# Optimization experiments

Measured on AMD Instinct MI355X. Metric: run time of the kernel, lower is better.

## Reference

```python
import jax, jax.numpy as jnp
import numpy as np

N_NODES = 50000
N_EDGES = 800000
IN_C, HID_C, OUT_C = 256, 128, 64
NUM_LAYERS = 3


def _glorot(key, shape):
    fan_in, fan_out = shape[0], shape[1]
    lim = np.sqrt(6.0 / (fan_in + fan_out)).astype(np.float32)
    return jax.random.uniform(key, shape, jnp.float32, -lim, lim)


def setup_inputs() -> dict:
    key = jax.random.key(0)
    ks = jax.random.split(key, 16)
    inp = {
        "x": jax.random.normal(ks[0], (N_NODES, IN_C), jnp.float32),
        "edge_index": jax.random.randint(ks[1], (2, N_EDGES), 0, N_NODES, jnp.int64),
        "proj_W": _glorot(ks[2], (IN_C, HID_C)),
        "proj_b": jnp.zeros((HID_C,), jnp.float32),
        "conv_W0": _glorot(ks[3], (HID_C, HID_C)),
        "conv_b0": jnp.zeros((HID_C,), jnp.float32),
        "conv_W1": _glorot(ks[4], (HID_C, HID_C)),
        "conv_b1": jnp.zeros((HID_C,), jnp.float32),
        "conv_W2": _glorot(ks[5], (HID_C, HID_C)),
        "conv_b2": jnp.zeros((HID_C,), jnp.float32),
        "out_W": _glorot(ks[6], (HID_C, OUT_C)),
        "out_b": jnp.zeros((OUT_C,), jnp.float32),
    }
    return inp


def _gcn_conv(h, W, b, src, dst, norm):
    # GCNConv: transform, then normalized scatter-add aggregation (self-loops
    # are already folded into src/dst/norm).
    h = h @ W                                   # [N, hid]
    msg = h[src] * norm[:, None]                # [E+N, hid] gather + scale
    agg = jax.ops.segment_sum(msg, dst, num_segments=N_NODES)
    return agg + b


def reference(x, edge_index, proj_W, proj_b, conv_W0, conv_b0, conv_W1,
              conv_b1, conv_W2, conv_b2, out_W, out_b):
    # Add self-loops once (same structure every layer).
    loop = jnp.arange(N_NODES, dtype=edge_index.dtype)
    src = jnp.concatenate([edge_index[0], loop])
    dst = jnp.concatenate([edge_index[1], loop])
    # Symmetric normalization: deg computed on destinations incl. self-loops.
    deg = jax.ops.segment_sum(jnp.ones_like(dst, dtype=x.dtype), dst,
                              num_segments=N_NODES)
    dis = jnp.where(deg > 0, jax.lax.rsqrt(deg), 0.0)
    norm = dis[src] * dis[dst]

    h = x @ proj_W + proj_b
    for W, b in ((conv_W0, conv_b0), (conv_W1, conv_b1), (conv_W2, conv_b2)):
        h = jax.nn.relu(_gcn_conv(h, W, b, src, dst, norm))
        # dropout is identity in eval mode
    return h @ out_W + out_b
```

## Files before the change

### kernel.cpp

```cpp
#include <hip/hip_runtime.h>
#include <hip/hip_bf16.h>

#define N_NODES 50000
#define N_EDGES 800000
#define IN_C 256
#define HID_C 128
#define OUT_C 64

#define N_BINS ((N_NODES + 127) / 128)
#define N_TOT (N_EDGES + N_NODES)

#define RB_BLOCK 1024
#define RB_EPT 8
#define RB_CHUNK (RB_BLOCK * RB_EPT)
#define RB_GRID ((N_TOT + RB_CHUNK - 1) / RB_CHUNK)

typedef __attribute__((ext_vector_type(8))) short bf16x8;
typedef __attribute__((ext_vector_type(4))) float f32x4;
typedef __attribute__((ext_vector_type(2))) _Float16 f16x2;

__device__ __forceinline__ ushort f2bf(float f) {
    uint u = __float_as_uint(f);
    u += 0x7fff + ((u >> 16) & 1);
    return (ushort)(u >> 16);
}
__device__ __forceinline__ float bf2f(ushort h) {
    return __uint_as_float(((uint)h) << 16);
}
__device__ __forceinline__ uint packhl(float v) {
    ushort h = f2bf(v);
    ushort l = f2bf(v - bf2f(h));
    return ((uint)h << 16) | (uint)l;
}


__global__ __launch_bounds__(256) void zero_binhist_kernel(int* __restrict__ binhist) {
    int i = blockIdx.x * 256 + threadIdx.x;
    if (i < N_BINS) binhist[i] = 0;
}

__global__ __launch_bounds__(256) void bin_hist_kernel(const int* __restrict__ dst,
                                                       int* __restrict__ binhist) {
    __shared__ int h[N_BINS];
    int t = threadIdx.x;
    for (int b = t; b < N_BINS; b += 256) h[b] = 0;
    __syncthreads();
    for (int i = blockIdx.x * 256 + t; i < N_EDGES; i += gridDim.x * 256)
        atomicAdd(&h[dst[i] >> 7], 1);
    __syncthreads();
    for (int b = t; b < N_BINS; b += 256)
        if (h[b]) atomicAdd(&binhist[b], h[b]);
}

__global__ __launch_bounds__(512) void bin_scan_kernel(const int* __restrict__ binhist,
                                                       int* __restrict__ bin_base,
                                                       int* __restrict__ bincur,
                                                       int* __restrict__ row_ptr) {
    __shared__ int s[512];
    int t = threadIdx.x;
    int v = 0;
    if (t < N_BINS) {
        int sl = (t == N_BINS - 1) ? (N_NODES - (N_BINS - 1) * 128) : 128;
        v = binhist[t] + sl;
    }
    s[t] = v;
    __syncthreads();
    for (int off = 1; off < 512; off <<= 1) {
        int x = s[t];
        int a = (t >= off) ? s[t - off] : 0;
        __syncthreads();
        s[t] = x + a;
        __syncthreads();
    }
    if (t < N_BINS) {
        bin_base[t] = s[t] - v;
        bincur[t] = 0;
    }
    if (t == N_BINS - 1) bin_base[N_BINS] = s[t];
    if (t == 0) row_ptr[N_NODES] = N_TOT;
}

__global__ __launch_bounds__(RB_BLOCK) void bin_scatter_kernel(
    const int* __restrict__ src, const int* __restrict__ dst,
    const int* __restrict__ bin_base, int* __restrict__ bincur,
    uint* __restrict__ binned) {
    __shared__ int hist[N_BINS];
    __shared__ int cur[N_BINS];
    const int t = threadIdx.x;
    for (int b = t; b < N_BINS; b += RB_BLOCK) hist[b] = 0;
    __syncthreads();

    uint pk[RB_EPT];
    int bn[RB_EPT];
    const int base = blockIdx.x * RB_CHUNK;
#pragma unroll
    for (int k = 0; k < RB_EPT; k++) {
        int i = base + k * RB_BLOCK + t;
        bn[k] = -1;
        if (i < N_TOT) {
            int s, d;
            if (i < N_EDGES) {
                s = src[i];
                d = dst[i];
            } else {
                s = d = i - N_EDGES;
            }
            pk[k] = (uint)s | ((uint)d << 16);
            bn[k] = d >> 7;
            atomicAdd(&hist[bn[k]], 1);
        }
    }
    __syncthreads();

    for (int b = t; b < N_BINS; b += RB_BLOCK) {
        int c = hist[b];
        int g0 = (c > 0) ? atomicAdd(&bincur[b], c) : 0;
        cur[b] = bin_base[b] + g0;
    }
    __syncthreads();

#pragma unroll
    for (int k = 0; k < RB_EPT; k++) {
        if (bn[k] >= 0) {
            int pos = atomicAdd(&cur[bn[k]], 1);
            binned[pos] = pk[k];
        }
    }
}

__global__ __launch_bounds__(256) void csr_build_kernel(const uint* __restrict__ binned,
                                                        const int* __restrict__ bin_base,
                                                        int* __restrict__ row_ptr,
                                                        float* __restrict__ dis,
                                                        ushort* __restrict__ csr_src) {
    __shared__ int hist[128];
    __shared__ int sc[256];
    __shared__ int exs[128];
    __shared__ int cur[128];
    const int b = blockIdx.x;
    const int t = threadIdx.x;
    const int start = bin_base[b];
    const int cnt = bin_base[b + 1] - start;
    const int nloc = min(128, N_NODES - b * 128);

    if (t < 128) hist[t] = 0;
    __syncthreads();
    for (int i = t; i < cnt; i += 256) {
        uint e = binned[start + i];
        atomicAdd(&hist[(e >> 16) & 127], 1);
    }
    __syncthreads();
    sc[t] = (t < 128) ? hist[t] : 0;
    __syncthreads();
    for (int off = 1; off < 128; off <<= 1) {
        int x = sc[t];
        int a = (t >= off) ? sc[t - off] : 0;
        __syncthreads();
        sc[t] = x + a;
        __syncthreads();
    }
    if (t < 128) {
        exs[t] = sc[t] - hist[t];
        cur[t] = 0;
    }
    __syncthreads();
    if (t < nloc) {
        row_ptr[b * 128 + t] = start + exs[t];
        dis[b * 128 + t] = rsqrtf((float)hist[t]);
    }
    for (int i = t; i < cnt; i += 256) {
        uint e = binned[start + i];
        int dl = (e >> 16) & 127;
        int pos = start + exs[dl] + atomicAdd(&cur[dl], 1);
        csr_src[pos] = (ushort)(e & 0xFFFFu);
    }
}


__device__ __forceinline__ void pack_w_body(const float* W, ushort* Ph, ushort* Pl,
                                            int K, int N, int bb, int lane) {
    int CT = N / 16;
    int ct = bb % CT;
    int kt = bb / CT;
    int lr = lane & 15, lg = lane >> 4;
    size_t base = ((size_t)bb * 64 + lane) * 8;
#pragma unroll
    for (int j = 0; j < 8; j++) {
        float w = W[(size_t)(kt * 32 + lg * 8 + j) * N + ct * 16 + lr];
        ushort h = f2bf(w);
        ushort lo = f2bf(w - bf2f(h));
        Ph[base + j] = h;
        Pl[base + j] = lo;
    }
}

__global__ __launch_bounds__(64) void pack_all_kernel(
    const float* __restrict__ projW, const float* __restrict__ W0,
    const float* __restrict__ W1, const float* __restrict__ W2,
    const float* __restrict__ outW,
    ushort* __restrict__ Pph, ushort* __restrict__ Ppl,
    ushort* __restrict__ P0h, ushort* __restrict__ P0l,
    ushort* __restrict__ P1h, ushort* __restrict__ P1l,
    ushort* __restrict__ P2h, ushort* __restrict__ P2l,
    ushort* __restrict__ Poh, ushort* __restrict__ Pol) {
    int b = blockIdx.x;
    int lane = threadIdx.x;
    if (b < 64) {
        pack_w_body(projW, Pph, Ppl, IN_C, HID_C, b, lane);
    } else if (b < 160) {
        int l = (b - 64) >> 5;
        int bb = (b - 64) & 31;
        const float* W = (l == 0) ? W0 : (l == 1) ? W1 : W2;
        ushort* Ph = (l == 0) ? P0h : (l == 1) ? P1h : P2h;
        ushort* Pl = (l == 0) ? P0l : (l == 1) ? P1l : P2l;
        pack_w_body(W, Ph, Pl, HID_C, HID_C, bb, lane);
    } else {
        pack_w_body(outW, Poh, Pol, HID_C, OUT_C, b - 160, lane);
    }
}


template <int K, int N, int OUT_MODE>
__global__ __launch_bounds__(256) void gemm_mfma_kernel(
    const uint* __restrict__ Ax, const ushort* __restrict__ Wph,
    const ushort* __restrict__ Wpl, const float* __restrict__ bias,
    float* __restrict__ Cf, int M) {
    constexpr int CT_TOT = N / 16;
    constexpr int NWC = CT_TOT / 4;
    constexpr int NWR = 4 / NWC;
    constexpr int KT = K / 32;
    constexpr int MT = 2;
    constexpr int RPB = NWR * MT * 16;

    const int wid = threadIdx.x >> 6;
    const int lane = threadIdx.x & 63;
    const int lr = lane & 15;
    const int lg = lane >> 4;
    const int wr = (NWC == 1) ? wid : (wid >> 1);
    const int wc = (NWC == 1) ? 0 : (wid & 1);
    const int row_base = blockIdx.x * RPB + wr * (MT * 16);
    const int ct0 = wc * 4;

    f32x4 acc[MT][4];
#pragma unroll
    for (int mt = 0; mt < MT; mt++)
#pragma unroll
        for (int ct = 0; ct < 4; ct++) acc[mt][ct] = (f32x4){0.f, 0.f, 0.f, 0.f};

    int rr_[MT];
#pragma unroll
    for (int mt = 0; mt < MT; mt++) {
        int r = row_base + mt * 16 + lr;
        rr_[mt] = (r >= M) ? (M - 1) : r;
    }

    uint4 apk[KT][MT][2];
#pragma unroll
    for (int kt = 0; kt < KT; kt++)
#pragma unroll
        for (int mt = 0; mt < MT; mt++) {
            const uint* ab = &Ax[(size_t)rr_[mt] * K + lg * 8];
            apk[kt][mt][0] = *(const uint4*)(ab + kt * 32);
            apk[kt][mt][1] = *(const uint4*)(ab + kt * 32 + 4);
        }

#pragma unroll
    for (int kt = 0; kt < KT; kt++) {
        const ushort* bh = &Wph[((size_t)kt * CT_TOT + ct0) * 512 + (size_t)lane * 8];
        const ushort* bl = &Wpl[((size_t)kt * CT_TOT + ct0) * 512 + (size_t)lane * 8];
        bf16x8 bhv[4], blv[4];
#pragma unroll
        for (int ct = 0; ct < 4; ct++) {
            bhv[ct] = *(const bf16x8*)(bh + ct * 512);
            blv[ct] = *(const bf16x8*)(bl + ct * 512);
        }

        bf16x8 ah[MT], al[MT];
#pragma unroll
        for (int mt = 0; mt < MT; mt++) {
            union { uint u[4]; bf16x8 v; } ch_, cl_;
#pragma unroll
            for (int j = 0; j < 4; j++) {
                uint u0 = (j < 2) ? ((const uint*)&apk[kt][mt][0])[j * 2]
                                  : ((const uint*)&apk[kt][mt][1])[(j - 2) * 2];
                uint u1 = (j < 2) ? ((const uint*)&apk[kt][mt][0])[j * 2 + 1]
                                  : ((const uint*)&apk[kt][mt][1])[(j - 2) * 2 + 1];
                ch_.u[j] = (u0 >> 16) | (u1 & 0xFFFF0000u);
                cl_.u[j] = (u0 & 0xFFFFu) | (u1 << 16);
            }
            ah[mt] = ch_.v;
            al[mt] = cl_.v;
        }

#pragma unroll
        for (int mt = 0; mt < MT; mt++)
#pragma unroll
            for (int ct = 0; ct < 4; ct++) {
                acc[mt][ct] = __builtin_amdgcn_mfma_f32_16x16x32_bf16(ah[mt], bhv[ct], acc[mt][ct], 0, 0, 0);
                acc[mt][ct] = __builtin_amdgcn_mfma_f32_16x16x32_bf16(al[mt], bhv[ct], acc[mt][ct], 0, 0, 0);
                acc[mt][ct] = __builtin_amdgcn_mfma_f32_16x16x32_bf16(ah[mt], blv[ct], acc[mt][ct], 0, 0, 0);
            }
    }

#pragma unroll
    for (int mt = 0; mt < MT; mt++)
#pragma unroll
        for (int ct = 0; ct < 4; ct++)
#pragma unroll
            for (int j = 0; j < 4; j++) {
                int rr = row_base + mt * 16 + lg * 4 + j;
                if (rr >= M) continue;
                int c = (ct0 + ct) * 16 + lr;
                Cf[(size_t)rr * N + c] = acc[mt][ct][j] + bias[c];
            }
}


__global__ __launch_bounds__(256) void proj_gemm_lds_kernel(
    const float* __restrict__ Af, const ushort* __restrict__ Wph,
    const ushort* __restrict__ Wpl, const float* __restrict__ bias,
    uint* __restrict__ Cx, int M) {
    __shared__ float As[64][132];

    const int t = threadIdx.x;
    const int r0 = blockIdx.x * 64;

    float4 pf[8];
#pragma unroll
    for (int i = 0; i < 8; i++) {
        int slot = i * 256 + t;
        int row = slot >> 5;
        int c4 = (slot & 31) << 2;
        int gr = r0 + row;
        if (gr >= M) gr = M - 1;
        float4 v0 = *(const float4*)&Af[(size_t)gr * IN_C + c4];
        pf[i] = *(const float4*)&Af[(size_t)gr * IN_C + 128 + c4];
        *(float4*)&As[row][c4] = v0;
    }
    __syncthreads();

    const int wid = t >> 6;
    const int lane = t & 63;
    const int lr = lane & 15;
    const int lg = lane >> 4;
    const int wr = wid >> 1;
    const int wc = wid & 1;
    const int ct0 = wc * 4;

    f32x4 acc[2][4];
#pragma unroll
    for (int mt = 0; mt < 2; mt++)
#pragma unroll
        for (int ct = 0; ct < 4; ct++) acc[mt][ct] = (f32x4){0.f, 0.f, 0.f, 0.f};

#pragma unroll
    for (int half = 0; half < 2; half++) {
#pragma unroll
        for (int kk = 0; kk < 4; kk++) {
            const int kt = half * 4 + kk;
            const ushort* bh = &Wph[((size_t)kt * 8 + ct0) * 512 + (size_t)lane * 8];
            const ushort* bl = &Wpl[((size_t)kt * 8 + ct0) * 512 + (size_t)lane * 8];
            bf16x8 bhv[4], blv[4];
#pragma unroll
            for (int ct = 0; ct < 4; ct++) {
                bhv[ct] = *(const bf16x8*)(bh + ct * 512);
                blv[ct] = *(const bf16x8*)(bl + ct * 512);
            }

            bf16x8 ah[2], al[2];
#pragma unroll
            for (int mt = 0; mt < 2; mt++) {
                int row = wr * 32 + mt * 16 + lr;
                float4 a0 = *(const float4*)&As[row][kk * 32 + lg * 8];
                float4 a1 = *(const float4*)&As[row][kk * 32 + lg * 8 + 4];
                float av[8] = {a0.x, a0.y, a0.z, a0.w, a1.x, a1.y, a1.z, a1.w};
#pragma unroll
                for (int j = 0; j < 8; j++) {
                    ushort h = f2bf(av[j]);
                    ushort lo = f2bf(av[j] - bf2f(h));
                    ah[mt][j] = (short)h;
                    al[mt][j] = (short)lo;
                }
            }

#pragma unroll
            for (int mt = 0; mt < 2; mt++)
#pragma unroll
                for (int ct = 0; ct < 4; ct++) {
                    acc[mt][ct] = __builtin_amdgcn_mfma_f32_16x16x32_bf16(ah[mt], bhv[ct], acc[mt][ct], 0, 0, 0);
                    acc[mt][ct] = __builtin_amdgcn_mfma_f32_16x16x32_bf16(al[mt], bhv[ct], acc[mt][ct], 0, 0, 0);
                    acc[mt][ct] = __builtin_amdgcn_mfma_f32_16x16x32_bf16(ah[mt], blv[ct], acc[mt][ct], 0, 0, 0);
                }
        }
        if (half == 0) {
            __syncthreads();
#pragma unroll
            for (int i = 0; i < 8; i++) {
                int slot = i * 256 + t;
                int row = slot >> 5;
                int c4 = (slot & 31) << 2;
                *(float4*)&As[row][c4] = pf[i];
            }
            __syncthreads();
        }
    }

#pragma unroll
    for (int mt = 0; mt < 2; mt++)
#pragma unroll
        for (int ct = 0; ct < 4; ct++)
#pragma unroll
            for (int j = 0; j < 4; j++) {
                int rr = r0 + wr * 32 + mt * 16 + lg * 4 + j;
                if (rr >= M) continue;
                int c = (ct0 + ct) * 16 + lr;
                Cx[(size_t)rr * HID_C + c] = packhl(acc[mt][ct][j] + bias[c]);
            }
}


__global__ __launch_bounds__(256) void conv_gemm_lds_kernel(
    const uint* __restrict__ Ax, const ushort* __restrict__ Wph,
    const ushort* __restrict__ Wpl, const float* __restrict__ disp,
    _Float16* __restrict__ Ch, int M) {
    constexpr int KT = 4;
    __shared__ uint As[64][132];

    const int t = threadIdx.x;
    const int r0 = blockIdx.x * 64;

#pragma unroll
    for (int i = 0; i < 8; i++) {
        int slot = i * 256 + t;
        int row = slot >> 5;
        int c16 = (slot & 31) << 2;
        int gr = r0 + row;
        if (gr >= M) gr = M - 1;
        uint4 v = *(const uint4*)&Ax[(size_t)gr * HID_C + c16];
        *(uint4*)&As[row][c16] = v;
    }
    __syncthreads();

    const int wid = t >> 6;
    const int lane = t & 63;
    const int lr = lane & 15;
    const int lg = lane >> 4;
    const int wr = wid >> 1;
    const int wc = wid & 1;
    const int ct0 = wc * 4;

    f32x4 acc[2][4];
#pragma unroll
    for (int mt = 0; mt < 2; mt++)
#pragma unroll
        for (int ct = 0; ct < 4; ct++) acc[mt][ct] = (f32x4){0.f, 0.f, 0.f, 0.f};

#pragma unroll
    for (int kt = 0; kt < KT; kt++) {
        const ushort* bh = &Wph[((size_t)kt * 8 + ct0) * 512 + (size_t)lane * 8];
        const ushort* bl = &Wpl[((size_t)kt * 8 + ct0) * 512 + (size_t)lane * 8];
        bf16x8 bhv[4], blv[4];
#pragma unroll
        for (int ct = 0; ct < 4; ct++) {
            bhv[ct] = *(const bf16x8*)(bh + ct * 512);
            blv[ct] = *(const bf16x8*)(bl + ct * 512);
        }

        bf16x8 ah[2], al[2];
#pragma unroll
        for (int mt = 0; mt < 2; mt++) {
            int row = wr * 32 + mt * 16 + lr;
            uint4 a0 = *(const uint4*)&As[row][kt * 32 + lg * 8];
            uint4 a1 = *(const uint4*)&As[row][kt * 32 + lg * 8 + 4];
            union { uint u[4]; bf16x8 v; } ch_, cl_;
            const uint* w0 = (const uint*)&a0;
            const uint* w1 = (const uint*)&a1;
#pragma unroll
            for (int j = 0; j < 4; j++) {
                uint u0 = (j < 2) ? w0[j * 2] : w1[(j - 2) * 2];
                uint u1 = (j < 2) ? w0[j * 2 + 1] : w1[(j - 2) * 2 + 1];
                ch_.u[j] = (u0 >> 16) | (u1 & 0xFFFF0000u);
                cl_.u[j] = (u0 & 0xFFFFu) | (u1 << 16);
            }
            ah[mt] = ch_.v;
            al[mt] = cl_.v;
        }

#pragma unroll
        for (int mt = 0; mt < 2; mt++)
#pragma unroll
            for (int ct = 0; ct < 4; ct++) {
                acc[mt][ct] = __builtin_amdgcn_mfma_f32_16x16x32_bf16(ah[mt], bhv[ct], acc[mt][ct], 0, 0, 0);
                acc[mt][ct] = __builtin_amdgcn_mfma_f32_16x16x32_bf16(al[mt], bhv[ct], acc[mt][ct], 0, 0, 0);
                acc[mt][ct] = __builtin_amdgcn_mfma_f32_16x16x32_bf16(ah[mt], blv[ct], acc[mt][ct], 0, 0, 0);
            }
    }

#pragma unroll
    for (int mt = 0; mt < 2; mt++)
#pragma unroll
        for (int ct = 0; ct < 4; ct++)
#pragma unroll
            for (int j = 0; j < 4; j++) {
                int rr = r0 + wr * 32 + mt * 16 + lg * 4 + j;
                if (rr >= M) continue;
                int c = (ct0 + ct) * 16 + lr;
                Ch[(size_t)rr * HID_C + c] = (_Float16)(acc[mt][ct][j] * disp[rr]);
            }
}


__global__ __launch_bounds__(256) void aggregate_kernel(const _Float16* __restrict__ g,
                                                        const int* __restrict__ row_ptr,
                                                        const ushort* __restrict__ csr_src,
                                                        const float* __restrict__ dis,
                                                        const float* __restrict__ bias,
                                                        uint* __restrict__ hx) {
    const int wid = threadIdx.x >> 6;
    const int lane = threadIdx.x & 63;
    const int node = blockIdx.x * 4 + wid;
    if (node >= N_NODES) return;
    const int c2 = lane * 2;

    const int s0 = row_ptr[node];
    const int s1 = row_ptr[node + 1];

    float ax = 0.f, ay = 0.f;
    int e = s0;
    for (; e + 16 <= s1; e += 16) {
        int idx[16];
#pragma unroll
        for (int j = 0; j < 16; j++) idx[j] = csr_src[e + j];
        f16x2 v[16];
#pragma unroll
        for (int j = 0; j < 16; j++)
            v[j] = *(const f16x2*)&g[(size_t)idx[j] * HID_C + c2];
        float sx = 0.f, sy = 0.f;
#pragma unroll
        for (int j = 0; j < 16; j++) {
            sx += (float)v[j].x;
            sy += (float)v[j].y;
        }
        ax += sx;
        ay += sy;
    }
    for (; e + 4 <= s1; e += 4) {
        int idx[4];
#pragma unroll
        for (int j = 0; j < 4; j++) idx[j] = csr_src[e + j];
        f16x2 v[4];
#pragma unroll
        for (int j = 0; j < 4; j++)
            v[j] = *(const f16x2*)&g[(size_t)idx[j] * HID_C + c2];
        ax += ((float)v[0].x + (float)v[1].x) + ((float)v[2].x + (float)v[3].x);
        ay += ((float)v[0].y + (float)v[1].y) + ((float)v[2].y + (float)v[3].y);
    }
    for (; e < s1; e++) {
        int i0 = csr_src[e];
        f16x2 v0 = *(const f16x2*)&g[(size_t)i0 * HID_C + c2];
        ax += (float)v0.x;
        ay += (float)v0.y;
    }

    const float dn = dis[node];
    float2 bb = *(const float2*)&bias[c2];
    float vx = fmaxf(dn * ax + bb.x, 0.f);
    float vy = fmaxf(dn * ay + bb.y, 0.f);
    uint2 w;
    w.x = packhl(vx);
    w.y = packhl(vy);
    *(uint2*)&hx[(size_t)node * HID_C + c2] = w;
}


extern "C" void kernel_launch(void* const* d_in, const int* in_sizes, int n_in,
                              void* d_out, int out_size, void* d_ws, size_t ws_size,
                              hipStream_t stream) {
    const float* x       = (const float*)d_in[0];
    const int*   eidx    = (const int*)d_in[1];
    const float* proj_W  = (const float*)d_in[2];
    const float* proj_b  = (const float*)d_in[3];
    const float* conv_W0 = (const float*)d_in[4];
    const float* conv_b0 = (const float*)d_in[5];
    const float* conv_W1 = (const float*)d_in[6];
    const float* conv_b1 = (const float*)d_in[7];
    const float* conv_W2 = (const float*)d_in[8];
    const float* conv_b2 = (const float*)d_in[9];
    const float* out_W   = (const float*)d_in[10];
    const float* out_b   = (const float*)d_in[11];
    float* out = (float*)d_out;

    const int* src = eidx;
    const int* dst = eidx + N_EDGES;

    char* ws = (char*)d_ws;
    size_t off = 0;
    auto carve = [&](size_t bytes) {
        void* p = ws + off;
        off += (bytes + 255) & ~(size_t)255;
        return p;
    };
    int*    row_ptr  = (int*)carve((N_NODES + 1) * sizeof(int));
    ushort* csr_src  = (ushort*)carve((size_t)N_TOT * sizeof(ushort));
    uint*   binned   = (uint*)carve((size_t)N_TOT * sizeof(uint));
    int*    binhist  = (int*)carve(N_BINS * sizeof(int));
    int*    bin_base = (int*)carve((N_BINS + 1) * sizeof(int));
    int*    bincur   = (int*)carve(N_BINS * sizeof(int));
    float*  dis      = (float*)carve(N_NODES * sizeof(float));
    ushort* projPh = (ushort*)carve((size_t)IN_C * HID_C * sizeof(ushort));
    ushort* projPl = (ushort*)carve((size_t)IN_C * HID_C * sizeof(ushort));
    ushort* convPh[3], *convPl[3];
    for (int l = 0; l < 3; l++) {
        convPh[l] = (ushort*)carve((size_t)HID_C * HID_C * sizeof(ushort));
        convPl[l] = (ushort*)carve((size_t)HID_C * HID_C * sizeof(ushort));
    }
    ushort* outPh = (ushort*)carve((size_t)HID_C * OUT_C * sizeof(ushort));
    ushort* outPl = (ushort*)carve((size_t)HID_C * OUT_C * sizeof(ushort));
    uint*   hx = (uint*)carve((size_t)N_NODES * HID_C * sizeof(uint));
    _Float16* g = (_Float16*)carve((size_t)N_NODES * HID_C * sizeof(_Float16));

    zero_binhist_kernel<<<(N_BINS + 255) / 256, 256, 0, stream>>>(binhist);
    bin_hist_kernel<<<196, 256, 0, stream>>>(dst, binhist);
    bin_scan_kernel<<<1, 512, 0, stream>>>(binhist, bin_base, bincur, row_ptr);
    bin_scatter_kernel<<<RB_GRID, RB_BLOCK, 0, stream>>>(
        src, dst, bin_base, bincur, binned);
    csr_build_kernel<<<N_BINS, 256, 0, stream>>>(
        binned, bin_base, row_ptr, dis, csr_src);

    pack_all_kernel<<<176, 64, 0, stream>>>(proj_W, conv_W0, conv_W1, conv_W2, out_W,
                                            projPh, projPl,
                                            convPh[0], convPl[0],
                                            convPh[1], convPl[1],
                                            convPh[2], convPl[2],
                                            outPh, outPl);

    const int grid_n128 = (N_NODES + 63) / 64;
    const int grid_n64  = (N_NODES + 127) / 128;
    const int agg_grid  = (N_NODES + 3) / 4;

    proj_gemm_lds_kernel<<<grid_n128, 256, 0, stream>>>(
        x, projPh, projPl, proj_b, hx, N_NODES);

    ushort* Wh_[3] = {convPh[0], convPh[1], convPh[2]};
    ushort* Wl_[3] = {convPl[0], convPl[1], convPl[2]};
    const float* bs_[3] = {conv_b0, conv_b1, conv_b2};
    for (int l = 0; l < 3; l++) {
        conv_gemm_lds_kernel<<<grid_n128, 256, 0, stream>>>(
            hx, Wh_[l], Wl_[l], dis, g, N_NODES);
        aggregate_kernel<<<agg_grid, 256, 0, stream>>>(
            g, row_ptr, csr_src, dis, bs_[l], hx);
    }

    gemm_mfma_kernel<HID_C, OUT_C, 0><<<grid_n64, 256, 0, stream>>>(
        hx, outPh, outPl, out_b, out, N_NODES);
}
```

Baseline: 245.9 us.

## Use register-pipelined projection GEMM and LDS-staged output GEMM

The projection GEMM no longer stages x through LDS with barriers. Each lane now loads its A fragments straight from global memory into a 3-deep rotating register prefetch buffer and converts fp32 to split bf16 hi/lo in registers. The output GEMM gets its own kernel: 128-thread blocks of 64 rows cooperatively stage the packed activations into LDS with coalesced loads, then each wave handles 32 rows across all 64 output columns. The goal is fewer barriers and better load coalescing, at the cost of more live registers and less coalesced direct global reads in the projection.

```diff
diff --git a/kernel.cpp b/kernel.cpp
--- a/kernel.cpp
+++ b/kernel.cpp
@@ -220,25 +220,21 @@
 }
 
 
-template <int K, int N, int OUT_MODE>
-__global__ __launch_bounds__(256) void gemm_mfma_kernel(
-    const uint* __restrict__ Ax, const ushort* __restrict__ Wph,
+__global__ __launch_bounds__(256) void proj_gemm_kernel(
+    const float* __restrict__ Af, const ushort* __restrict__ Wph,
     const ushort* __restrict__ Wpl, const float* __restrict__ bias,
-    float* __restrict__ Cf, int M) {
-    constexpr int CT_TOT = N / 16;
-    constexpr int NWC = CT_TOT / 4;
-    constexpr int NWR = 4 / NWC;
-    constexpr int KT = K / 32;
+    uint* __restrict__ Cx, int M) {
+    constexpr int KT = IN_C / 32;
     constexpr int MT = 2;
-    constexpr int RPB = NWR * MT * 16;
+    constexpr int AD = 3;
 
     const int wid = threadIdx.x >> 6;
     const int lane = threadIdx.x & 63;
     const int lr = lane & 15;
     const int lg = lane >> 4;
-    const int wr = (NWC == 1) ? wid : (wid >> 1);
-    const int wc = (NWC == 1) ? 0 : (wid & 1);
-    const int row_base = blockIdx.x * RPB + wr * (MT * 16);
+    const int wr = wid >> 1;
+    const int wc = wid & 1;
+    const int row_base = blockIdx.x * 64 + wr * 32;
     const int ct0 = wc * 4;
 
     f32x4 acc[MT][4];
@@ -254,20 +250,20 @@
         rr_[mt] = (r >= M) ? (M - 1) : r;
     }
 
-    uint4 apk[KT][MT][2];
-#pragma unroll
-    for (int kt = 0; kt < KT; kt++)
+    float4 va[AD][MT][2];
+#pragma unroll
+    for (int p = 0; p < AD; p++)
 #pragma unroll
         for (int mt = 0; mt < MT; mt++) {
-            const uint* ab = &Ax[(size_t)rr_[mt] * K + lg * 8];
-            apk[kt][mt][0] = *(const uint4*)(ab + kt * 32);
-            apk[kt][mt][1] = *(const uint4*)(ab + kt * 32 + 4);
+            const float* ap = &Af[(size_t)rr_[mt] * IN_C + p * 32 + lg * 8];
+            va[p][mt][0] = *(const float4*)ap;
+            va[p][mt][1] = *(const float4*)(ap + 4);
         }
 
 #pragma unroll
     for (int kt = 0; kt < KT; kt++) {
-        const ushort* bh = &Wph[((size_t)kt * CT_TOT + ct0) * 512 + (size_t)lane * 8];
-        const ushort* bl = &Wpl[((size_t)kt * CT_TOT + ct0) * 512 + (size_t)lane * 8];
+        const ushort* bh = &Wph[((size_t)kt * 8 + ct0) * 512 + (size_t)lane * 8];
+        const ushort* bl = &Wpl[((size_t)kt * 8 + ct0) * 512 + (size_t)lane * 8];
         bf16x8 bhv[4], blv[4];
 #pragma unroll
         for (int ct = 0; ct < 4; ct++) {
@@ -276,20 +272,26 @@
         }
 
         bf16x8 ah[MT], al[MT];
+        const int cb = kt % AD;
 #pragma unroll
         for (int mt = 0; mt < MT; mt++) {
-            union { uint u[4]; bf16x8 v; } ch_, cl_;
-#pragma unroll
-            for (int j = 0; j < 4; j++) {
-                uint u0 = (j < 2) ? ((const uint*)&apk[kt][mt][0])[j * 2]
-                                  : ((const uint*)&apk[kt][mt][1])[(j - 2) * 2];
-                uint u1 = (j < 2) ? ((const uint*)&apk[kt][mt][0])[j * 2 + 1]
-                                  : ((const uint*)&apk[kt][mt][1])[(j - 2) * 2 + 1];
-                ch_.u[j] = (u0 >> 16) | (u1 & 0xFFFF0000u);
-                cl_.u[j] = (u0 & 0xFFFFu) | (u1 << 16);
-            }
-            ah[mt] = ch_.v;
-            al[mt] = cl_.v;
+            float av[8] = {va[cb][mt][0].x, va[cb][mt][0].y, va[cb][mt][0].z, va[cb][mt][0].w,
+                           va[cb][mt][1].x, va[cb][mt][1].y, va[cb][mt][1].z, va[cb][mt][1].w};
+#pragma unroll
+            for (int j = 0; j < 8; j++) {
+                ushort h = f2bf(av[j]);
+                ushort lo = f2bf(av[j] - bf2f(h));
+                ah[mt][j] = (short)h;
+                al[mt][j] = (short)lo;
+            }
+        }
+        if (kt + AD < KT) {
+#pragma unroll
+            for (int mt = 0; mt < MT; mt++) {
+                const float* ap = &Af[(size_t)rr_[mt] * IN_C + (kt + AD) * 32 + lg * 8];
+                va[cb][mt][0] = *(const float4*)ap;
+                va[cb][mt][1] = *(const float4*)(ap + 4);
+            }
         }
 
 #pragma unroll
@@ -309,109 +311,6 @@
 #pragma unroll
             for (int j = 0; j < 4; j++) {
                 int rr = row_base + mt * 16 + lg * 4 + j;
-                if (rr >= M) continue;
-                int c = (ct0 + ct) * 16 + lr;
-                Cf[(size_t)rr * N + c] = acc[mt][ct][j] + bias[c];
-            }
-}
-
-
-__global__ __launch_bounds__(256) void proj_gemm_lds_kernel(
-    const float* __restrict__ Af, const ushort* __restrict__ Wph,
-    const ushort* __restrict__ Wpl, const float* __restrict__ bias,
-    uint* __restrict__ Cx, int M) {
-    __shared__ float As[64][132];
-
-    const int t = threadIdx.x;
-    const int r0 = blockIdx.x * 64;
-
-    float4 pf[8];
-#pragma unroll
-    for (int i = 0; i < 8; i++) {
-        int slot = i * 256 + t;
-        int row = slot >> 5;
-        int c4 = (slot & 31) << 2;
-        int gr = r0 + row;
-        if (gr >= M) gr = M - 1;
-        float4 v0 = *(const float4*)&Af[(size_t)gr * IN_C + c4];
-        pf[i] = *(const float4*)&Af[(size_t)gr * IN_C + 128 + c4];
-        *(float4*)&As[row][c4] = v0;
-    }
-    __syncthreads();
-
-    const int wid = t >> 6;
-    const int lane = t & 63;
-    const int lr = lane & 15;
-    const int lg = lane >> 4;
-    const int wr = wid >> 1;
-    const int wc = wid & 1;
-    const int ct0 = wc * 4;
-
-    f32x4 acc[2][4];
-#pragma unroll
-    for (int mt = 0; mt < 2; mt++)
-#pragma unroll
-        for (int ct = 0; ct < 4; ct++) acc[mt][ct] = (f32x4){0.f, 0.f, 0.f, 0.f};
-
-#pragma unroll
-    for (int half = 0; half < 2; half++) {
-#pragma unroll
-        for (int kk = 0; kk < 4; kk++) {
-            const int kt = half * 4 + kk;
-            const ushort* bh = &Wph[((size_t)kt * 8 + ct0) * 512 + (size_t)lane * 8];
-            const ushort* bl = &Wpl[((size_t)kt * 8 + ct0) * 512 + (size_t)lane * 8];
-            bf16x8 bhv[4], blv[4];
-#pragma unroll
-            for (int ct = 0; ct < 4; ct++) {
-                bhv[ct] = *(const bf16x8*)(bh + ct * 512);
-                blv[ct] = *(const bf16x8*)(bl + ct * 512);
-            }
-
-            bf16x8 ah[2], al[2];
-#pragma unroll
-            for (int mt = 0; mt < 2; mt++) {
-                int row = wr * 32 + mt * 16 + lr;
-                float4 a0 = *(const float4*)&As[row][kk * 32 + lg * 8];
-                float4 a1 = *(const float4*)&As[row][kk * 32 + lg * 8 + 4];
-                float av[8] = {a0.x, a0.y, a0.z, a0.w, a1.x, a1.y, a1.z, a1.w};
-#pragma unroll
-                for (int j = 0; j < 8; j++) {
-                    ushort h = f2bf(av[j]);
-                    ushort lo = f2bf(av[j] - bf2f(h));
-                    ah[mt][j] = (short)h;
-                    al[mt][j] = (short)lo;
-                }
-            }
-
-#pragma unroll
-            for (int mt = 0; mt < 2; mt++)
-#pragma unroll
-                for (int ct = 0; ct < 4; ct++) {
-                    acc[mt][ct] = __builtin_amdgcn_mfma_f32_16x16x32_bf16(ah[mt], bhv[ct], acc[mt][ct], 0, 0, 0);
-                    acc[mt][ct] = __builtin_amdgcn_mfma_f32_16x16x32_bf16(al[mt], bhv[ct], acc[mt][ct], 0, 0, 0);
-                    acc[mt][ct] = __builtin_amdgcn_mfma_f32_16x16x32_bf16(ah[mt], blv[ct], acc[mt][ct], 0, 0, 0);
-                }
-        }
-        if (half == 0) {
-            __syncthreads();
-#pragma unroll
-            for (int i = 0; i < 8; i++) {
-                int slot = i * 256 + t;
-                int row = slot >> 5;
-                int c4 = (slot & 31) << 2;
-                *(float4*)&As[row][c4] = pf[i];
-            }
-            __syncthreads();
-        }
-    }
-
-#pragma unroll
-    for (int mt = 0; mt < 2; mt++)
-#pragma unroll
-        for (int ct = 0; ct < 4; ct++)
-#pragma unroll
-            for (int j = 0; j < 4; j++) {
-                int rr = r0 + wr * 32 + mt * 16 + lg * 4 + j;
                 if (rr >= M) continue;
                 int c = (ct0 + ct) * 16 + lr;
                 Cx[(size_t)rr * HID_C + c] = packhl(acc[mt][ct][j] + bias[c]);
@@ -506,6 +405,94 @@
                 if (rr >= M) continue;
                 int c = (ct0 + ct) * 16 + lr;
                 Ch[(size_t)rr * HID_C + c] = (_Float16)(acc[mt][ct][j] * disp[rr]);
+            }
+}
+
+
+__global__ __launch_bounds__(128) void out_gemm_lds_kernel(
+    const uint* __restrict__ Ax, const ushort* __restrict__ Wph,
+    const ushort* __restrict__ Wpl, const float* __restrict__ bias,
+    float* __restrict__ Cf, int M) {
+    constexpr int KT = 4;
+    __shared__ uint As[64][132];
+
+    const int t = threadIdx.x;
+    const int r0 = blockIdx.x * 64;
+
+#pragma unroll
+    for (int i = 0; i < 16; i++) {
+        int slot = i * 128 + t;
+        int row = slot >> 5;
+        int c16 = (slot & 31) << 2;
+        int gr = r0 + row;
+        if (gr >= M) gr = M - 1;
+        uint4 v = *(const uint4*)&Ax[(size_t)gr * HID_C + c16];
+        *(uint4*)&As[row][c16] = v;
+    }
+    __syncthreads();
+
+    const int wid = t >> 6;
+    const int lane = t & 63;
+    const int lr = lane & 15;
+    const int lg = lane >> 4;
+
+    f32x4 acc[2][4];
+#pragma unroll
+    for (int mt = 0; mt < 2; mt++)
+#pragma unroll
+        for (int ct = 0; ct < 4; ct++) acc[mt][ct] = (f32x4){0.f, 0.f, 0.f, 0.f};
+
+#pragma unroll
+    for (int kt = 0; kt < KT; kt++) {
+        const ushort* bh = &Wph[(size_t)kt * 4 * 512 + (size_t)lane * 8];
+        const ushort* bl = &Wpl[(size_t)kt * 4 * 512 + (size_t)lane * 8];
+        bf16x8 bhv[4], blv[4];
+#pragma unroll
+        for (int ct = 0; ct < 4; ct++) {
+            bhv[ct] = *(const bf16x8*)(bh + ct * 512);
+            blv[ct] = *(const bf16x8*)(bl + ct * 512);
+        }
+
+        bf16x8 ah[2], al[2];
+#pragma unroll
+        for (int mt = 0; mt < 2; mt++) {
+            int row = wid * 32 + mt * 16 + lr;
+            uint4 a0 = *(const uint4*)&As[row][kt * 32 + lg * 8];
+            uint4 a1 = *(const uint4*)&As[row][kt * 32 + lg * 8 + 4];
+            union { uint u[4]; bf16x8 v; } ch_, cl_;
+            const uint* w0 = (const uint*)&a0;
+            const uint* w1 = (const uint*)&a1;
+#pragma unroll
+            for (int j = 0; j < 4; j++) {
+                uint u0 = (j < 2) ? w0[j * 2] : w1[(j - 2) * 2];
+                uint u1 = (j < 2) ? w0[j * 2 + 1] : w1[(j - 2) * 2 + 1];
+                ch_.u[j] = (u0 >> 16) | (u1 & 0xFFFF0000u);
+                cl_.u[j] = (u0 & 0xFFFFu) | (u1 << 16);
+            }
+            ah[mt] = ch_.v;
+            al[mt] = cl_.v;
+        }
+
+#pragma unroll
+        for (int mt = 0; mt < 2; mt++)
+#pragma unroll
+            for (int ct = 0; ct < 4; ct++) {
+                acc[mt][ct] = __builtin_amdgcn_mfma_f32_16x16x32_bf16(ah[mt], bhv[ct], acc[mt][ct], 0, 0, 0);
+                acc[mt][ct] = __builtin_amdgcn_mfma_f32_16x16x32_bf16(al[mt], bhv[ct], acc[mt][ct], 0, 0, 0);
+                acc[mt][ct] = __builtin_amdgcn_mfma_f32_16x16x32_bf16(ah[mt], blv[ct], acc[mt][ct], 0, 0, 0);
+            }
+    }
+
+#pragma unroll
+    for (int mt = 0; mt < 2; mt++)
+#pragma unroll
+        for (int ct = 0; ct < 4; ct++)
+#pragma unroll
+            for (int j = 0; j < 4; j++) {
+                int rr = r0 + wid * 32 + mt * 16 + lg * 4 + j;
+                if (rr >= M) continue;
+                int c = ct * 16 + lr;
+                Cf[(size_t)rr * OUT_C + c] = acc[mt][ct][j] + bias[c];
             }
 }
 
@@ -635,10 +622,9 @@
                                             outPh, outPl);
 
     const int grid_n128 = (N_NODES + 63) / 64;
-    const int grid_n64  = (N_NODES + 127) / 128;
     const int agg_grid  = (N_NODES + 3) / 4;
 
-    proj_gemm_lds_kernel<<<grid_n128, 256, 0, stream>>>(
+    proj_gemm_kernel<<<grid_n128, 256, 0, stream>>>(
         x, projPh, projPl, proj_b, hx, N_NODES);
 
     ushort* Wh_[3] = {convPh[0], convPh[1], convPh[2]};
@@ -651,6 +637,6 @@
             g, row_ptr, csr_src, dis, bs_[l], hx);
     }
 
-    gemm_mfma_kernel<HID_C, OUT_C, 0><<<grid_n64, 256, 0, stream>>>(
+    out_gemm_lds_kernel<<<grid_n128, 128, 0, stream>>>(
         hx, outPh, outPl, out_b, out, N_NODES);
 }
```

Result: no change. 242.3 us (median of 2 runs) (-1.4%).
